# Kernel tuning notes

Hardware: AMD Instinct MI355X
Metric: run time of the kernel (lower is better)

Reference implementation:

```python
import jax, jax.numpy as jnp
import numpy as np

B, C_IN, S = 32, 4, 2048
NF = 256          # CNN filters
H = 256           # LSTM hidden per direction
NH, DH = 8, 64    # heads, single-head size
MH = 512          # multihead size
KSZ, PAD, POOL = 13, 6, 6
SP = (S + 2 * PAD - KSZ + 1) // POOL  # 341: post conv(len-preserving)+maxpool1d length


def _lstm_dir(x, Wih, Whh, b):
    # x: [T, N, C] -- torch LSTM gate order i,f,g,o; b = b_ih + b_hh merged
    N = x.shape[1]
    h0 = jnp.zeros((N, H), x.dtype)
    c0 = jnp.zeros((N, H), x.dtype)

    def step(carry, xt):
        h, c = carry
        g = xt @ Wih.T + h @ Whh.T + b
        i, f, gg, o = jnp.split(g, 4, axis=-1)
        c = jax.nn.sigmoid(f) * c + jax.nn.sigmoid(i) * jnp.tanh(gg)
        h = jax.nn.sigmoid(o) * jnp.tanh(c)
        return (h, c), h

    _, hs = jax.lax.scan(step, (h0, c0), x)
    return hs


def _bilstm(x, Wih, Whh, b):
    fwd = _lstm_dir(x, Wih[0], Whh[0], b[0])
    bwd = _lstm_dir(x[::-1], Wih[1], Whh[1], b[1])[::-1]
    return jnp.concatenate([fwd, bwd], axis=-1)


def _rpe():
    # RelativePosition: |clip(k-q, -(S-1), S-1)| / (S-1); identical across the
    # batch-repeat channels, so compute once then broadcast (same math).
    r = jnp.arange(S)
    d = jnp.abs(jnp.clip(r[None, :] - r[:, None], -(S - 1), S - 1))
    d = d.astype(jnp.float32) / jnp.float32(S - 1)
    # nn.MaxPool2d((9,9), stride=(6,6), padding=1) -> [341, 341]
    return jax.lax.reduce_window(d, -jnp.inf, jax.lax.max, (9, 9), (6, 6), [(1, 1), (1, 1)])


def setup_inputs():
    key = jax.random.key(0)
    ks = jax.random.split(key, 20)
    f = lambda i, shape: jax.random.normal(ks[i], shape, jnp.float32) * 0.05
    return {
        "inputs": jax.random.normal(ks[0], (B, C_IN, S), jnp.float32),
        "conv1_w": f(1, (NF, C_IN, KSZ)),
        "bn1_gamma": jnp.ones((NF,), jnp.float32),
        "bn1_beta": jnp.zeros((NF,), jnp.float32),
        "Wih0": f(2, (2, 4 * H, NF)),
        "Whh0": f(3, (2, 4 * H, H)),
        "b0": f(4, (2, 4 * H)),
        "Wih1": f(5, (2, 4 * H, 2 * H)),
        "Whh1": f(6, (2, 4 * H, H)),
        "b1": f(7, (2, 4 * H)),
        "Qw": f(8, (NH, DH, 2 * H)), "Qb": f(9, (NH, DH)),
        "Kw": f(10, (NH, DH, 2 * H)), "Kb": f(11, (NH, DH)),
        "Vw": f(12, (NH, DH, 2 * H)), "Vb": f(13, (NH, DH)),
        "mh_w": f(14, (MH, NH * DH)), "mh_b": f(15, (MH,)),
    }


def reference(inputs, conv1_w, bn1_gamma, bn1_beta, Wih0, Whh0, b0,
              Wih1, Whh1, b1, Qw, Qb, Kw, Kb, Vw, Vb, mh_w, mh_b):
    # layer1: Conv1d (bias=False, pad=6 keeps length) + BatchNorm1d(eval: mean=0, var=1) + ReLU + MaxPool1d(6)
    x = jax.lax.conv_general_dilated(inputs, conv1_w, (1,), [(PAD, PAD)],
                                     dimension_numbers=('NCH', 'OIH', 'NCH'))
    x = x * (bn1_gamma / jnp.sqrt(1.0 + 1e-5))[None, :, None] + bn1_beta[None, :, None]
    x = jax.nn.relu(x)
    x = jax.lax.reduce_window(x, -jnp.inf, jax.lax.max, (1, 1, POOL), (1, 1, POOL), 'VALID')  # [B,NF,SP]
    x = jnp.transpose(x, (0, 2, 1))  # [B, SP, NF]

    # torch nn.LSTM with batch_first=False fed [B,SP,NF]: scans over axis 0 (batch) -- replicated faithfully.
    x = _bilstm(x, Wih0, Whh0, b0)
    x = _bilstm(x, Wih1, Whh1, b1)  # [B, SP, 2H]
    # (the F_RNN/R_RNN split-and-concat is an identity)

    # per-head Q/K/V (batched over heads), relative attention, dropout off (eval)
    q = jnp.einsum('bsc,hdc->hbsd', x, Qw) + Qb[:, None, None, :]
    k = jnp.einsum('bsc,hdc->hbsd', x, Kw) + Kb[:, None, None, :]
    v = jnp.einsum('bsc,hdc->hbsd', x, Vw) + Vb[:, None, None, :]
    scores = jnp.einsum('hbqd,hbkd->hbqk', q, k) / jnp.sqrt(jnp.float32(DH))
    scores = scores / _rpe()[None, None, :, :]
    p = jax.nn.softmax(scores, axis=-1)
    attn = jax.nn.relu(jnp.einsum('hbqk,hbkd->hbqd', p, v))  # [NH,B,SP,DH]
    cat = jnp.transpose(attn, (1, 2, 0, 3)).reshape(B, SP, NH * DH)
    out = jax.nn.relu(cat @ mh_w.T + mh_b)  # MultiHeadLinear + MHReLU
    return out
```

## Files before the change

kernel.cpp:

```cpp
#include <hip/hip_runtime.h>
#include <math.h>

#define B_    32
#define CIN   4
#define SLEN  2048
#define NF    256
#define HD    256
#define SP    341
#define RTOT  (B_*SP)
#define NH_   8
#define DH_   64
#define GRP   4
#define HS    (SP*HD)
#define PKS   768
#define BSTR  136

typedef __attribute__((ext_vector_type(8))) short short8;
typedef __attribute__((ext_vector_type(4))) float floatx4;
typedef __attribute__((ext_vector_type(4))) unsigned short ushortx4;
typedef __attribute__((ext_vector_type(8))) unsigned short ushort8;

__device__ __forceinline__ float sigmoidf_(float x) { return 1.0f / (1.0f + expf(-x)); }

__device__ __forceinline__ unsigned short f2bf(float x) {
    unsigned int u = __float_as_uint(x);
    unsigned int r = (u + 0x7FFF + ((u >> 16) & 1)) >> 16;
    return (unsigned short)r;
}
__device__ __forceinline__ float bf2f(unsigned short b) {
    return __uint_as_float(((unsigned int)b) << 16);
}

__device__ __forceinline__ void store_f4_llc(float* p, floatx4 v)
{
    asm volatile("global_store_dwordx4 %0, %1, off sc0 sc1" :: "v"(p), "v"(v) : "memory");
}
__device__ __forceinline__ unsigned load_u32_llc(const unsigned* p)
{
    unsigned r;
    asm volatile("global_load_dword %0, %1, off sc0 sc1\n\ts_waitcnt vmcnt(0)"
                 : "=v"(r) : "v"(p) : "memory");
    return r;
}
__device__ __forceinline__ void load_h16_llc(const float* p, floatx4* r)
{
    asm volatile(
        "global_load_dwordx4 %0, %16, off sc0 sc1\n\t"
        "global_load_dwordx4 %1, %16, off offset:16 sc0 sc1\n\t"
        "global_load_dwordx4 %2, %16, off offset:128 sc0 sc1\n\t"
        "global_load_dwordx4 %3, %16, off offset:144 sc0 sc1\n\t"
        "global_load_dwordx4 %4, %16, off offset:256 sc0 sc1\n\t"
        "global_load_dwordx4 %5, %16, off offset:272 sc0 sc1\n\t"
        "global_load_dwordx4 %6, %16, off offset:384 sc0 sc1\n\t"
        "global_load_dwordx4 %7, %16, off offset:400 sc0 sc1\n\t"
        "global_load_dwordx4 %8, %16, off offset:512 sc0 sc1\n\t"
        "global_load_dwordx4 %9, %16, off offset:528 sc0 sc1\n\t"
        "global_load_dwordx4 %10, %16, off offset:640 sc0 sc1\n\t"
        "global_load_dwordx4 %11, %16, off offset:656 sc0 sc1\n\t"
        "global_load_dwordx4 %12, %16, off offset:768 sc0 sc1\n\t"
        "global_load_dwordx4 %13, %16, off offset:784 sc0 sc1\n\t"
        "global_load_dwordx4 %14, %16, off offset:896 sc0 sc1\n\t"
        "global_load_dwordx4 %15, %16, off offset:912 sc0 sc1\n\t"
        "s_waitcnt vmcnt(0)"
        : "=&v"(r[0]), "=&v"(r[1]), "=&v"(r[2]), "=&v"(r[3]),
          "=&v"(r[4]), "=&v"(r[5]), "=&v"(r[6]), "=&v"(r[7]),
          "=&v"(r[8]), "=&v"(r[9]), "=&v"(r[10]), "=&v"(r[11]),
          "=&v"(r[12]), "=&v"(r[13]), "=&v"(r[14]), "=&v"(r[15])
        : "v"(p)
        : "memory");
}


__global__ __launch_bounds__(256)
void conv_pool_k(const float* __restrict__ in, const float* __restrict__ cw,
                 const float* __restrict__ gamma, const float* __restrict__ beta,
                 unsigned short* __restrict__ x0p)
{
    const int b  = blockIdx.y;
    const int s0 = blockIdx.x * 16;
    const int co = threadIdx.x;
    __shared__ float ins[CIN][16*6 + 12];
    for (int idx = threadIdx.x; idx < CIN*108; idx += 256) {
        int ci = idx / 108, o = idx % 108;
        int pos = 6*s0 - 6 + o;
        ins[ci][o] = (pos >= 0 && pos < SLEN) ? in[(b*CIN + ci)*SLEN + pos] : 0.0f;
    }
    float wreg[52];
    {
        const float4* wp = (const float4*)(cw + co*52);
        #pragma unroll
        for (int j4 = 0; j4 < 13; ++j4) {
            float4 w4 = wp[j4];
            wreg[j4*4+0]=w4.x; wreg[j4*4+1]=w4.y; wreg[j4*4+2]=w4.z; wreg[j4*4+3]=w4.w;
        }
    }
    const float scale = gamma[co] * (1.0f / sqrtf(1.0f + 1e-5f));
    const float shift = beta[co];
    __syncthreads();
    for (int si = 0; si < 16; ++si) {
        int s = s0 + si;
        if (s >= SP) break;
        float win[CIN][18];
        #pragma unroll
        for (int ci = 0; ci < CIN; ++ci)
            #pragma unroll
            for (int o = 0; o < 18; ++o)
                win[ci][o] = ins[ci][6*si + o];
        float m = -1e30f;
        #pragma unroll
        for (int p6 = 0; p6 < 6; ++p6) {
            float acc = 0.0f;
            #pragma unroll
            for (int ci = 0; ci < CIN; ++ci)
                #pragma unroll
                for (int kk = 0; kk < 13; ++kk)
                    acc += win[ci][p6+kk] * wreg[ci*13+kk];
            float val = acc * scale + shift;
            val = fmaxf(val, 0.0f);
            m = fmaxf(m, val);
        }
        unsigned short hb_ = f2bf(m);
        unsigned short lb_ = f2bf(m - bf2f(hb_));
        size_t rb = (size_t)(b*SP + s)*512 + (size_t)(co >> 3)*16 + (co & 7);
        x0p[rb]     = hb_;
        x0p[rb + 8] = lb_;
    }
}

__global__ __launch_bounds__(256)
void pack4_k(const float* __restrict__ W, unsigned short* __restrict__ hi,
             unsigned short* __restrict__ lo, int n4)
{
    int i = blockIdx.x * 256 + threadIdx.x;
    if (i >= n4) return;
    float4 x = *((const float4*)W + i);
    float v[4] = {x.x, x.y, x.z, x.w};
    ushortx4 h, l;
    #pragma unroll
    for (int e = 0; e < 4; ++e) {
        unsigned short hb = f2bf(v[e]);
        h[e] = hb;
        l[e] = f2bf(v[e] - bf2f(hb));
    }
    *((ushortx4*)hi + i) = h;
    *((ushortx4*)lo + i) = l;
}

__global__ __launch_bounds__(256)
void pack8_k(const float* __restrict__ W, unsigned short* __restrict__ O, int n8)
{
    int i = blockIdx.x * 256 + threadIdx.x;
    if (i >= n8) return;
    const float4* wp = (const float4*)W + (size_t)i*2;
    float4 a = wp[0], b = wp[1];
    float v[8] = {a.x,a.y,a.z,a.w,b.x,b.y,b.z,b.w};
    ushort8 h, l;
    #pragma unroll
    for (int e = 0; e < 8; ++e) {
        unsigned short hb = f2bf(v[e]);
        h[e] = hb;
        l[e] = f2bf(v[e] - bf2f(hb));
    }
    *(ushort8*)(O + (size_t)i*16)     = h;
    *(ushort8*)(O + (size_t)i*16 + 8) = l;
}

template<int RELU>
__global__ __launch_bounds__(256)
void gemm_bf_k(const unsigned short* __restrict__ Ap, const unsigned short* __restrict__ Bp,
               const float* __restrict__ bias, float* __restrict__ C,
               int M, int N, int K)
{
    const int n0 = blockIdx.x * 128;
    const int m0 = blockIdx.y * 128;
    const int tid = threadIdx.x;
    const int lane = tid & 63;
    const int w = tid >> 6;
    const int wm = w >> 1, wn = w & 1;
    const int ln15 = lane & 15, lq = lane >> 4;
    const int l8 = lane >> 3, lj = lane & 7;
    const size_t rstr = 2*(size_t)K;

    __shared__ unsigned short As[128*64];
    __shared__ unsigned short Bs[128*64];

    floatx4 acc[4][4];
    #pragma unroll
    for (int i = 0; i < 4; ++i)
        #pragma unroll
        for (int j = 0; j < 4; ++j) acc[i][j] = (floatx4){0.f, 0.f, 0.f, 0.f};

    int rloc[4];
    #pragma unroll
    for (int c = 0; c < 4; ++c) rloc[c] = w*32 + c*8 + l8;
    const int spos = lj ^ (l8 & 7);

    for (int k0 = 0; k0 < K; k0 += 32) {
        short8 va[4], vb[4];
        #pragma unroll
        for (int c = 0; c < 4; ++c) {
            int gra = m0 + rloc[c]; if (gra >= M) gra = M - 1;
            va[c] = *(const short8*)(Ap + (size_t)gra*rstr + k0*2 + lj*8);
            vb[c] = *(const short8*)(Bp + (size_t)(n0 + rloc[c])*rstr + k0*2 + lj*8);
        }
        __syncthreads();
        #pragma unroll
        for (int c = 0; c < 4; ++c) {
            *(short8*)&As[rloc[c]*64 + spos*8] = va[c];
            *(short8*)&Bs[rloc[c]*64 + spos*8] = vb[c];
        }
        __syncthreads();

        short8 fa_h[4], fa_l[4], fb_h[4], fb_l[4];
        #pragma unroll
        for (int mt = 0; mt < 4; ++mt) {
            const int lr = wm*64 + mt*16 + ln15;
            fa_h[mt] = *(const short8*)&As[lr*64 + (((lq*2  ) ^ (lr&7))*8)];
            fa_l[mt] = *(const short8*)&As[lr*64 + (((lq*2+1) ^ (lr&7))*8)];
        }
        #pragma unroll
        for (int nt = 0; nt < 4; ++nt) {
            const int lr = wn*64 + nt*16 + ln15;
            fb_h[nt] = *(const short8*)&Bs[lr*64 + (((lq*2  ) ^ (lr&7))*8)];
            fb_l[nt] = *(const short8*)&Bs[lr*64 + (((lq*2+1) ^ (lr&7))*8)];
        }
        #pragma unroll
        for (int mt = 0; mt < 4; ++mt)
            #pragma unroll
            for (int nt = 0; nt < 4; ++nt) {
                acc[mt][nt] = __builtin_amdgcn_mfma_f32_16x16x32_bf16(fa_l[mt], fb_h[nt], acc[mt][nt], 0, 0, 0);
                acc[mt][nt] = __builtin_amdgcn_mfma_f32_16x16x32_bf16(fa_h[mt], fb_l[nt], acc[mt][nt], 0, 0, 0);
                acc[mt][nt] = __builtin_amdgcn_mfma_f32_16x16x32_bf16(fa_h[mt], fb_h[nt], acc[mt][nt], 0, 0, 0);
            }
    }

    #pragma unroll
    for (int nt = 0; nt < 4; ++nt) {
        const int n = n0 + wn*64 + nt*16 + ln15;
        const float bv = bias[n];
        #pragma unroll
        for (int mt = 0; mt < 4; ++mt) {
            const int mbase = m0 + wm*64 + mt*16 + lq*4;
            #pragma unroll
            for (int r = 0; r < 4; ++r) {
                int m = mbase + r;
                if (m < M) {
                    float val = acc[mt][nt][r] + bv;
                    if (RELU) val = fmaxf(val, 0.0f);
                    C[(size_t)m*N + n] = val;
                }
            }
        }
    }
}

__global__ __launch_bounds__(256)
void lstm_scan_k(const float* __restrict__ G,
                 const unsigned short* __restrict__ Whi,
                 const unsigned short* __restrict__ Wlo,
                 float* __restrict__ hb,
                 unsigned short* __restrict__ x_out,
                 unsigned* __restrict__ bar)
{
    const int j0 = blockIdx.x * 32;
    const int m0 = blockIdx.y * 32;
    const int d  = blockIdx.z;
    const int tid = threadIdx.x;
    const int w = tid >> 6, lane = tid & 63;
    const int mhalf = w & 1, gpair = w >> 1;
    const int ln15 = lane & 15, lq = lane >> 4;
    const size_t hsz = (size_t)2*SP*HD;
    unsigned* gbar = bar + (size_t)(blockIdx.y*2 + blockIdx.z)*64;

    __shared__ float Csh[32][132];

    int am = m0 + mhalf*16 + ln15; if (am > SP-1) am = SP-1;
    const int akoff = lq * 8;

    const unsigned short* WhiD = Whi + (size_t)d*1024*256;
    const unsigned short* WloD = Wlo + (size_t)d*1024*256;
    int nrow[4];
    #pragma unroll
    for (int t = 0; t < 4; ++t)
        nrow[t] = (gpair*2 + (t>>1))*256 + j0 + (t&1)*16 + ln15;

    const int emloc = tid >> 3;
    const int ej4   = (tid & 7) * 4;
    const int em    = m0 + emloc;

    floatx4 creg = (floatx4){0.f, 0.f, 0.f, 0.f};

    for (int s = 0; s < B_; ++s) {
        const int t_in = d ? (B_ - 1 - s) : s;
        float* hbuf_in  = hb + (size_t)(s & 1)*hsz;
        float* hbuf_out = hb + (size_t)((s+1) & 1)*hsz;

        floatx4 acc[4];
        #pragma unroll
        for (int t = 0; t < 4; ++t) acc[t] = (floatx4){0.f, 0.f, 0.f, 0.f};

        if (s > 0) {
            const float* p = hbuf_in + (size_t)d*HS + (size_t)am*HD + akoff;
            floatx4 hr[16];
            load_h16_llc(p, hr);
            #pragma unroll
            for (int kk = 0; kk < 8; ++kk) {
                const int ko = kk*32 + akoff;
                float vv[8] = {hr[2*kk][0], hr[2*kk][1], hr[2*kk][2], hr[2*kk][3],
                               hr[2*kk+1][0], hr[2*kk+1][1], hr[2*kk+1][2], hr[2*kk+1][3]};
                short8 ahi, alo;
                #pragma unroll
                for (int e = 0; e < 8; ++e) {
                    unsigned short hb16 = f2bf(vv[e]);
                    ahi[e] = (short)hb16;
                    alo[e] = (short)f2bf(vv[e] - bf2f(hb16));
                }
                #pragma unroll
                for (int t = 0; t < 4; ++t) {
                    short8 bhi = *(const short8*)(WhiD + (size_t)nrow[t]*HD + ko);
                    short8 blo = *(const short8*)(WloD + (size_t)nrow[t]*HD + ko);
                    acc[t] = __builtin_amdgcn_mfma_f32_16x16x32_bf16(alo, bhi, acc[t], 0, 0, 0);
                    acc[t] = __builtin_amdgcn_mfma_f32_16x16x32_bf16(ahi, blo, acc[t], 0, 0, 0);
                    acc[t] = __builtin_amdgcn_mfma_f32_16x16x32_bf16(ahi, bhi, acc[t], 0, 0, 0);
                }
            }
        }

        #pragma unroll
        for (int t = 0; t < 4; ++t) {
            int col = gpair*64 + (t>>1)*32 + (t&1)*16 + ln15;
            int rb  = mhalf*16 + lq*4;
            #pragma unroll
            for (int r = 0; r < 4; ++r)
                Csh[rb + r][col] = acc[t][r];
        }
        __syncthreads();

        if (em < SP) {
            size_t gb = ((size_t)t_in*SP + em)*2048 + (size_t)d*1024 + j0 + ej4;
            float4 gi4 = *(const float4*)&G[gb];
            float4 gf4 = *(const float4*)&G[gb + 256];
            float4 gg4 = *(const float4*)&G[gb + 512];
            float4 go4 = *(const float4*)&G[gb + 768];
            float hv[4];
            #pragma unroll
            for (int e = 0; e < 4; ++e) {
                float gi = Csh[emloc][     ej4+e] + (&gi4.x)[e];
                float gf = Csh[emloc][32 + ej4+e] + (&gf4.x)[e];
                float gg = Csh[emloc][64 + ej4+e] + (&gg4.x)[e];
                float go = Csh[emloc][96 + ej4+e] + (&go4.x)[e];
                float cn = sigmoidf_(gf)*creg[e] + sigmoidf_(gi)*tanhf(gg);
                creg[e] = cn;
                hv[e] = sigmoidf_(go)*tanhf(cn);
            }
            size_t cbase = ((size_t)d*SP + em)*HD + j0 + ej4;
            floatx4 ho = (floatx4){hv[0], hv[1], hv[2], hv[3]};
            store_f4_llc(&hbuf_out[cbase], ho);
            const int colg = d*HD + j0 + ej4;
            size_t xb = ((size_t)t_in*SP + em)*1024 + (size_t)(colg >> 3)*16 + (colg & 7);
            ushortx4 xh, xl;
            #pragma unroll
            for (int e = 0; e < 4; ++e) {
                unsigned short hb16 = f2bf(hv[e]);
                xh[e] = hb16;
                xl[e] = f2bf(hv[e] - bf2f(hb16));
            }
            *(ushortx4*)&x_out[xb]     = xh;
            *(ushortx4*)&x_out[xb + 8] = xl;
        }

        if (s < B_ - 1) {
            asm volatile("s_waitcnt vmcnt(0)" ::: "memory");
            __syncthreads();
            if (tid == 0) {
                atomicAdd(gbar, 1u);
                const unsigned target = (unsigned)(s + 1) * 8u;
                while (load_u32_llc(gbar) < target)
                    __builtin_amdgcn_s_sleep(2);
            }
            __syncthreads();
        }
    }
}

__global__ __launch_bounds__(256)
void scores_sm_k(const float* __restrict__ q, const float* __restrict__ k,
                 unsigned short* __restrict__ Ppk, int g)
{
    const int h = blockIdx.z, bl = blockIdx.y, bg = g*GRP + bl;
    const int q0 = blockIdx.x * 32;
    const int tid = threadIdx.x;
    const int tx = tid & 15, ty = tid >> 4;
    __shared__ float qs[32][68];
    __shared__ float ks[64][68];
    {
        int jr = tid >> 3, c8 = (tid & 7) * 8;
        int qq = q0 + jr; if (qq > SP-1) qq = SP-1;
        const float* qp = &q[((size_t)bg*SP + qq)*512 + h*64 + c8];
        *(float4*)&qs[jr][c8]     = *(const float4*)qp;
        *(float4*)&qs[jr][c8 + 4] = *(const float4*)(qp + 4);
    }
    float sv[2][24];
    for (int kc = 0; kc < 6; ++kc) {
        __syncthreads();
        {
            int jr = tid >> 2, c16 = (tid & 3) * 16;
            int kr = kc*64 + jr; if (kr > SP-1) kr = SP-1;
            const float* kp = &k[((size_t)bg*SP + kr)*512 + h*64 + c16];
            #pragma unroll
            for (int u = 0; u < 4; ++u)
                *(float4*)&ks[jr][c16 + u*4] = *(const float4*)(kp + u*4);
        }
        __syncthreads();
        float a_[2][4] = {{0.f,0.f,0.f,0.f},{0.f,0.f,0.f,0.f}};
        for (int d4 = 0; d4 < 64; d4 += 4) {
            float4 a0 = *(const float4*)&qs[ty][d4];
            float4 a1 = *(const float4*)&qs[ty + 16][d4];
            float4 b[4];
            #pragma unroll
            for (int j = 0; j < 4; ++j) b[j] = *(const float4*)&ks[tx + 16*j][d4];
            #pragma unroll
            for (int j = 0; j < 4; ++j) {
                a_[0][j] += a0.x*b[j].x + a0.y*b[j].y + a0.z*b[j].z + a0.w*b[j].w;
                a_[1][j] += a1.x*b[j].x + a1.y*b[j].y + a1.z*b[j].z + a1.w*b[j].w;
            }
        }
        #pragma unroll
        for (int i = 0; i < 2; ++i)
            #pragma unroll
            for (int j = 0; j < 4; ++j) sv[i][kc*4 + j] = a_[i][j];
    }
    #pragma unroll
    for (int i = 0; i < 2; ++i) {
        const int qq = q0 + ty + 16*i;
        int r0 = 6*qq - 1; if (r0 < 0) r0 = 0;
        int r1 = 6*qq + 7; if (r1 > SLEN-1) r1 = SLEN-1;
        float m = -1e30f;
        #pragma unroll
        for (int jj = 0; jj < 24; ++jj) {
            const int col = (jj >> 2)*64 + (jj & 3)*16 + tx;
            float s;
            if (col < SP) {
                int c0 = 6*col - 1; if (c0 < 0) c0 = 0;
                int c1 = 6*col + 7;
                int dd1 = c1 - r0; if (dd1 < 0) dd1 = -dd1;
                int dd2 = r1 - c0; if (dd2 < 0) dd2 = -dd2;
                int den = dd1 > dd2 ? dd1 : dd2;
                s = (sv[i][jj] * 0.125f) * 2047.0f / (float)den;
            } else s = -1e30f;
            sv[i][jj] = s;
            m = fmaxf(m, s);
        }
        #pragma unroll
        for (int o = 1; o < 16; o <<= 1) m = fmaxf(m, __shfl_xor(m, o, 64));
        float sum = 0.0f;
        #pragma unroll
        for (int jj = 0; jj < 24; ++jj) {
            float v = expf(sv[i][jj] - m);
            sv[i][jj] = v;
            sum += v;
        }
        #pragma unroll
        for (int o = 1; o < 16; o <<= 1) sum += __shfl_xor(sum, o, 64);
        const float inv = 1.0f / sum;
        if (qq < SP) {
            const size_t pb = ((size_t)(h*GRP + bl)*SP + qq) * PKS;
            #pragma unroll
            for (int jj = 0; jj < 24; ++jj) {
                const int col = (jj >> 2)*64 + (jj & 3)*16 + tx;
                float p = sv[i][jj] * inv;
                unsigned short hb16 = f2bf(p);
                size_t pp = pb + (size_t)((col >> 3)*16 + (col & 7));
                Ppk[pp]     = hb16;
                Ppk[pp + 8] = f2bf(p - bf2f(hb16));
            }
        }
    }
}

__global__ __launch_bounds__(256)
void pv_bf_k(const unsigned short* __restrict__ Ppk, const float* __restrict__ vbuf,
             unsigned short* __restrict__ catp, int g)
{
    const int h = blockIdx.z, bl = blockIdx.y, bg = g*GRP + bl;
    const int q0 = blockIdx.x * 64;
    const int tid = threadIdx.x;
    const int lane = tid & 63, w = tid >> 6;
    const int ln15 = lane & 15, lq = lane >> 4;
    __shared__ unsigned short As[64][BSTR];
    __shared__ unsigned short Bs[64][BSTR];
    floatx4 acc[4];
    #pragma unroll
    for (int nt = 0; nt < 4; ++nt) acc[nt] = (floatx4){0.f,0.f,0.f,0.f};
    const size_t prow = (size_t)(h*GRP + bl)*SP;
    const int sr = tid >> 2;
    const int sa = (tid & 3) * 32;
    const int sd = (tid & 3) * 16;

    for (int chunk = 0; chunk < 6; ++chunk) {
        int qa = q0 + sr; if (qa > SP-1) qa = SP-1;
        const unsigned short* ap = Ppk + (prow + qa)*PKS + chunk*128 + sa;
        short8 a0 = *(const short8*)ap;
        short8 a1 = *(const short8*)(ap + 8);
        short8 a2 = *(const short8*)(ap + 16);
        short8 a3 = *(const short8*)(ap + 24);
        const int kr = chunk*64 + sr;
        float vv[16];
        if (kr < SP) {
            const float* vp = &vbuf[((size_t)bg*SP + kr)*512 + h*64 + sd];
            *(float4*)&vv[0]  = ((const float4*)vp)[0];
            *(float4*)&vv[4]  = ((const float4*)vp)[1];
            *(float4*)&vv[8]  = ((const float4*)vp)[2];
            *(float4*)&vv[12] = ((const float4*)vp)[3];
        } else {
            #pragma unroll
            for (int e = 0; e < 16; ++e) vv[e] = 0.0f;
        }
        __syncthreads();
        *(short8*)&As[sr][sa]      = a0;
        *(short8*)&As[sr][sa + 8]  = a1;
        *(short8*)&As[sr][sa + 16] = a2;
        *(short8*)&As[sr][sa + 24] = a3;
        {
            const int c = (sr >> 3)*16 + (sr & 7);
            #pragma unroll
            for (int e = 0; e < 16; ++e) {
                unsigned short hb16 = f2bf(vv[e]);
                Bs[sd + e][c]     = hb16;
                Bs[sd + e][c + 8] = f2bf(vv[e] - bf2f(hb16));
            }
        }
        __syncthreads();
        #pragma unroll
        for (int s = 0; s < 2; ++s) {
            const int ko = s*64 + lq*16;
            short8 fa_h = *(const short8*)&As[w*16 + ln15][ko];
            short8 fa_l = *(const short8*)&As[w*16 + ln15][ko + 8];
            #pragma unroll
            for (int nt = 0; nt < 4; ++nt) {
                short8 fb_h = *(const short8*)&Bs[nt*16 + ln15][ko];
                short8 fb_l = *(const short8*)&Bs[nt*16 + ln15][ko + 8];
                acc[nt] = __builtin_amdgcn_mfma_f32_16x16x32_bf16(fa_l, fb_h, acc[nt], 0, 0, 0);
                acc[nt] = __builtin_amdgcn_mfma_f32_16x16x32_bf16(fa_h, fb_l, acc[nt], 0, 0, 0);
                acc[nt] = __builtin_amdgcn_mfma_f32_16x16x32_bf16(fa_h, fb_h, acc[nt], 0, 0, 0);
            }
        }
    }
    #pragma unroll
    for (int nt = 0; nt < 4; ++nt) {
        const int colg = h*64 + nt*16 + ln15;
        #pragma unroll
        for (int r = 0; r < 4; ++r) {
            const int em = q0 + w*16 + lq*4 + r;
            if (em < SP) {
                float val = fmaxf(acc[nt][r], 0.0f);
                size_t xb = ((size_t)bg*SP + em)*1024 + (size_t)((colg >> 3)*16 + (colg & 7));
                unsigned short hb16 = f2bf(val);
                catp[xb]     = hb16;
                catp[xb + 8] = f2bf(val - bf2f(hb16));
            }
        }
    }
}

extern "C" void kernel_launch(void* const* d_in, const int* in_sizes, int n_in,
                              void* d_out, int out_size, void* d_ws, size_t ws_size,
                              hipStream_t stream)
{
    (void)in_sizes; (void)n_in; (void)out_size; (void)ws_size;
    const float* in    = (const float*)d_in[0];
    const float* cw    = (const float*)d_in[1];
    const float* gamma = (const float*)d_in[2];
    const float* beta  = (const float*)d_in[3];
    const float* Wih0  = (const float*)d_in[4];
    const float* Whh0  = (const float*)d_in[5];
    const float* b0    = (const float*)d_in[6];
    const float* Wih1  = (const float*)d_in[7];
    const float* Whh1  = (const float*)d_in[8];
    const float* b1    = (const float*)d_in[9];
    const float* Qw    = (const float*)d_in[10];
    const float* Qb    = (const float*)d_in[11];
    const float* Kw    = (const float*)d_in[12];
    const float* Kb    = (const float*)d_in[13];
    const float* Vw    = (const float*)d_in[14];
    const float* Vb    = (const float*)d_in[15];
    const float* mhw   = (const float*)d_in[16];
    const float* mhb   = (const float*)d_in[17];
    float* out = (float*)d_out;

    float* x0 = (float*)d_ws;
    float* G  = x0 + (size_t)RTOT*NF;
    float* x1 = G  + (size_t)RTOT*2048;
    float* x2 = x1 + (size_t)RTOT*512;
    float* hb = x2 + (size_t)RTOT*512;
    float* cb = hb + (size_t)2*2*SP*HD;

    float* qbuf = G;
    float* kbuf = G + (size_t)RTOT*512;
    float* vbuf = G + (size_t)2*RTOT*512;
    unsigned short* Ppk = (unsigned short*)(G + (size_t)3*RTOT*512);
    unsigned* bar = (unsigned*)cb;

    unsigned short* x0p = (unsigned short*)x0;
    unsigned short* whh1_hi = (unsigned short*)x0;
    unsigned short* whh1_lo = whh1_hi + (size_t)524288;
    unsigned short* qw_p = (unsigned short*)(x0 + (size_t)524288);
    unsigned short* kw_p = qw_p + (size_t)524288;
    unsigned short* vw_p = kw_p + (size_t)524288;
    unsigned short* mw_p = vw_p + (size_t)524288;
    unsigned short* wih0_p  = (unsigned short*)x2;
    unsigned short* wih1_p  = wih0_p + (size_t)1048576;
    unsigned short* whh0_hi = wih1_p + (size_t)2097152;
    unsigned short* whh0_lo = whh0_hi + (size_t)524288;
    unsigned short* x1p  = (unsigned short*)x1;
    unsigned short* catp = (unsigned short*)x1;
    unsigned short* x2p = (unsigned short*)x2;

    #define PACKGRID(n) dim3(((n) + 255) / 256)

    conv_pool_k<<<dim3(22, B_), 256, 0, stream>>>(in, cw, gamma, beta, x0p);
    pack8_k<<<PACKGRID(65536), 256, 0, stream>>>(Wih0, wih0_p, 65536);
    gemm_bf_k<0><<<dim3(16, 86), 256, 0, stream>>>(x0p, wih0_p, b0, G, RTOT, 2048, 256);
    pack4_k<<<PACKGRID(131072), 256, 0, stream>>>(Whh0, whh0_hi, whh0_lo, 131072);
    pack4_k<<<PACKGRID(131072), 256, 0, stream>>>(Whh1, whh1_hi, whh1_lo, 131072);
    pack8_k<<<PACKGRID(131072), 256, 0, stream>>>(Wih1, wih1_p, 131072);
    hipMemsetAsync(bar, 0, 22*64*sizeof(unsigned), stream);
    {
        const float* a0 = G; const unsigned short* a1 = whh0_hi; const unsigned short* a2 = whh0_lo;
        float* a3 = hb; unsigned short* a4 = x1p; unsigned* a5 = bar;
        void* kargs[] = {&a0, &a1, &a2, &a3, &a4, &a5};
        hipLaunchCooperativeKernel((void*)lstm_scan_k, dim3(8, 11, 2), dim3(256, 1, 1), kargs, 0, stream);
    }
    gemm_bf_k<0><<<dim3(16, 86), 256, 0, stream>>>(x1p, wih1_p, b1, G, RTOT, 2048, 512);
    hipMemsetAsync(bar, 0, 22*64*sizeof(unsigned), stream);
    {
        const float* a0 = G; const unsigned short* a1 = whh1_hi; const unsigned short* a2 = whh1_lo;
        float* a3 = hb; unsigned short* a4 = x2p; unsigned* a5 = bar;
        void* kargs[] = {&a0, &a1, &a2, &a3, &a4, &a5};
        hipLaunchCooperativeKernel((void*)lstm_scan_k, dim3(8, 11, 2), dim3(256, 1, 1), kargs, 0, stream);
    }
    pack8_k<<<PACKGRID(32768), 256, 0, stream>>>(Qw,  qw_p, 32768);
    pack8_k<<<PACKGRID(32768), 256, 0, stream>>>(Kw,  kw_p, 32768);
    pack8_k<<<PACKGRID(32768), 256, 0, stream>>>(Vw,  vw_p, 32768);
    pack8_k<<<PACKGRID(32768), 256, 0, stream>>>(mhw, mw_p, 32768);
    gemm_bf_k<0><<<dim3(4, 86), 256, 0, stream>>>(x2p, qw_p, Qb, qbuf, RTOT, 512, 512);
    gemm_bf_k<0><<<dim3(4, 86), 256, 0, stream>>>(x2p, kw_p, Kb, kbuf, RTOT, 512, 512);
    gemm_bf_k<0><<<dim3(4, 86), 256, 0, stream>>>(x2p, vw_p, Vb, vbuf, RTOT, 512, 512);
    for (int g = 0; g < B_/GRP; ++g) {
        scores_sm_k<<<dim3(11, GRP, NH_), 256, 0, stream>>>(qbuf, kbuf, Ppk, g);
        pv_bf_k    <<<dim3(6,  GRP, NH_), 256, 0, stream>>>(Ppk, vbuf, catp, g);
    }
    gemm_bf_k<1><<<dim3(4, 86), 256, 0, stream>>>(catp, mw_p, mhb, out, RTOT, 512, 512);
    #undef PACKGRID
}
```

Measured before the change: 1.697 ms.

## Fuse scores, softmax and PV into one attention kernel over all batches

Replaces the per-group scores_sm_k and pv_bf_k launch pairs (16 launches) with a single attn_k over the full batch. The kernel keeps softmax probabilities in shared memory, which removes the packed bf16 hi/lo probability buffer and its global round trip. PV is now computed with fp32 FMAs from LDS instead of split-bf16 MFMA. Tiles shrink to 16 queries per block, so K and V are reloaded more often and the PV step runs on scalar FP32 ALUs rather than matrix cores.

```diff
diff --git a/kernel.cpp b/kernel.cpp
--- a/kernel.cpp
+++ b/kernel.cpp
@@ -10,10 +10,8 @@
 #define RTOT  (B_*SP)
 #define NH_   8
 #define DH_   64
-#define GRP   4
 #define HS    (SP*HD)
-#define PKS   768
-#define BSTR  136
+#define SSTR  388
 
 typedef __attribute__((ext_vector_type(8))) short short8;
 typedef __attribute__((ext_vector_type(4))) float floatx4;
@@ -384,23 +382,24 @@
 }
 
 __global__ __launch_bounds__(256)
-void scores_sm_k(const float* __restrict__ q, const float* __restrict__ k,
-                 unsigned short* __restrict__ Ppk, int g)
-{
-    const int h = blockIdx.z, bl = blockIdx.y, bg = g*GRP + bl;
-    const int q0 = blockIdx.x * 32;
+void attn_k(const float* __restrict__ q, const float* __restrict__ k,
+            const float* __restrict__ v, unsigned short* __restrict__ catp)
+{
+    const int h = blockIdx.z, bg = blockIdx.y;
+    const int q0 = blockIdx.x * 16;
     const int tid = threadIdx.x;
     const int tx = tid & 15, ty = tid >> 4;
-    __shared__ float qs[32][68];
-    __shared__ float ks[64][68];
+    __shared__ float qs[16][68];
+    __shared__ float st[64][68];
+    __shared__ float S[16][SSTR];
+
     {
-        int jr = tid >> 3, c8 = (tid & 7) * 8;
+        int jr = tid >> 4, c4 = (tid & 15) * 4;
         int qq = q0 + jr; if (qq > SP-1) qq = SP-1;
-        const float* qp = &q[((size_t)bg*SP + qq)*512 + h*64 + c8];
-        *(float4*)&qs[jr][c8]     = *(const float4*)qp;
-        *(float4*)&qs[jr][c8 + 4] = *(const float4*)(qp + 4);
-    }
-    float sv[2][24];
+        *(float4*)&qs[jr][c4] = *(const float4*)&q[((size_t)bg*SP + qq)*512 + h*64 + c4];
+    }
+
+    float sv[24];
     for (int kc = 0; kc < 6; ++kc) {
         __syncthreads();
         {
@@ -409,30 +408,25 @@
             const float* kp = &k[((size_t)bg*SP + kr)*512 + h*64 + c16];
             #pragma unroll
             for (int u = 0; u < 4; ++u)
-                *(float4*)&ks[jr][c16 + u*4] = *(const float4*)(kp + u*4);
-        }
-        __syncthreads();
-        float a_[2][4] = {{0.f,0.f,0.f,0.f},{0.f,0.f,0.f,0.f}};
+                *(float4*)&st[jr][c16 + u*4] = *(const float4*)(kp + u*4);
+        }
+        __syncthreads();
+        float a_[4] = {0.f, 0.f, 0.f, 0.f};
         for (int d4 = 0; d4 < 64; d4 += 4) {
             float4 a0 = *(const float4*)&qs[ty][d4];
-            float4 a1 = *(const float4*)&qs[ty + 16][d4];
             float4 b[4];
             #pragma unroll
-            for (int j = 0; j < 4; ++j) b[j] = *(const float4*)&ks[tx + 16*j][d4];
-            #pragma unroll
-            for (int j = 0; j < 4; ++j) {
-                a_[0][j] += a0.x*b[j].x + a0.y*b[j].y + a0.z*b[j].z + a0.w*b[j].w;
-                a_[1][j] += a1.x*b[j].x + a1.y*b[j].y + a1.z*b[j].z + a1.w*b[j].w;
-            }
-        }
-        #pragma unroll
-        for (int i = 0; i < 2; ++i)
-            #pragma unroll
-            for (int j = 0; j < 4; ++j) sv[i][kc*4 + j] = a_[i][j];
-    }
-    #pragma unroll
-    for (int i = 0; i < 2; ++i) {
-        const int qq = q0 + ty + 16*i;
+            for (int j = 0; j < 4; ++j) b[j] = *(const float4*)&st[tx + 16*j][d4];
+            #pragma unroll
+            for (int j = 0; j < 4; ++j)
+                a_[j] += a0.x*b[j].x + a0.y*b[j].y + a0.z*b[j].z + a0.w*b[j].w;
+        }
+        #pragma unroll
+        for (int j = 0; j < 4; ++j) sv[kc*4 + j] = a_[j];
+    }
+
+    {
+        const int qq = q0 + ty;
         int r0 = 6*qq - 1; if (r0 < 0) r0 = 0;
         int r1 = 6*qq + 7; if (r1 > SLEN-1) r1 = SLEN-1;
         float m = -1e30f;
@@ -446,9 +440,9 @@
                 int dd1 = c1 - r0; if (dd1 < 0) dd1 = -dd1;
                 int dd2 = r1 - c0; if (dd2 < 0) dd2 = -dd2;
                 int den = dd1 > dd2 ? dd1 : dd2;
-                s = (sv[i][jj] * 0.125f) * 2047.0f / (float)den;
+                s = (sv[jj] * 0.125f) * 2047.0f / (float)den;
             } else s = -1e30f;
-            sv[i][jj] = s;
+            sv[jj] = s;
             m = fmaxf(m, s);
         }
         #pragma unroll
@@ -456,110 +450,54 @@
         float sum = 0.0f;
         #pragma unroll
         for (int jj = 0; jj < 24; ++jj) {
-            float v = expf(sv[i][jj] - m);
-            sv[i][jj] = v;
-            sum += v;
+            float vv_ = expf(sv[jj] - m);
+            sv[jj] = vv_;
+            sum += vv_;
         }
         #pragma unroll
         for (int o = 1; o < 16; o <<= 1) sum += __shfl_xor(sum, o, 64);
         const float inv = 1.0f / sum;
-        if (qq < SP) {
-            const size_t pb = ((size_t)(h*GRP + bl)*SP + qq) * PKS;
-            #pragma unroll
-            for (int jj = 0; jj < 24; ++jj) {
-                const int col = (jj >> 2)*64 + (jj & 3)*16 + tx;
-                float p = sv[i][jj] * inv;
-                unsigned short hb16 = f2bf(p);
-                size_t pp = pb + (size_t)((col >> 3)*16 + (col & 7));
-                Ppk[pp]     = hb16;
-                Ppk[pp + 8] = f2bf(p - bf2f(hb16));
-            }
-        }
-    }
-}
-
-__global__ __launch_bounds__(256)
-void pv_bf_k(const unsigned short* __restrict__ Ppk, const float* __restrict__ vbuf,
-             unsigned short* __restrict__ catp, int g)
-{
-    const int h = blockIdx.z, bl = blockIdx.y, bg = g*GRP + bl;
-    const int q0 = blockIdx.x * 64;
-    const int tid = threadIdx.x;
-    const int lane = tid & 63, w = tid >> 6;
-    const int ln15 = lane & 15, lq = lane >> 4;
-    __shared__ unsigned short As[64][BSTR];
-    __shared__ unsigned short Bs[64][BSTR];
-    floatx4 acc[4];
-    #pragma unroll
-    for (int nt = 0; nt < 4; ++nt) acc[nt] = (floatx4){0.f,0.f,0.f,0.f};
-    const size_t prow = (size_t)(h*GRP + bl)*SP;
-    const int sr = tid >> 2;
-    const int sa = (tid & 3) * 32;
-    const int sd = (tid & 3) * 16;
-
-    for (int chunk = 0; chunk < 6; ++chunk) {
-        int qa = q0 + sr; if (qa > SP-1) qa = SP-1;
-        const unsigned short* ap = Ppk + (prow + qa)*PKS + chunk*128 + sa;
-        short8 a0 = *(const short8*)ap;
-        short8 a1 = *(const short8*)(ap + 8);
-        short8 a2 = *(const short8*)(ap + 16);
-        short8 a3 = *(const short8*)(ap + 24);
-        const int kr = chunk*64 + sr;
-        float vv[16];
-        if (kr < SP) {
-            const float* vp = &vbuf[((size_t)bg*SP + kr)*512 + h*64 + sd];
-            *(float4*)&vv[0]  = ((const float4*)vp)[0];
-            *(float4*)&vv[4]  = ((const float4*)vp)[1];
-            *(float4*)&vv[8]  = ((const float4*)vp)[2];
-            *(float4*)&vv[12] = ((const float4*)vp)[3];
-        } else {
-            #pragma unroll
-            for (int e = 0; e < 16; ++e) vv[e] = 0.0f;
-        }
-        __syncthreads();
-        *(short8*)&As[sr][sa]      = a0;
-        *(short8*)&As[sr][sa + 8]  = a1;
-        *(short8*)&As[sr][sa + 16] = a2;
-        *(short8*)&As[sr][sa + 24] = a3;
+        #pragma unroll
+        for (int jj = 0; jj < 24; ++jj) {
+            const int col = (jj >> 2)*64 + (jj & 3)*16 + tx;
+            S[ty][col] = sv[jj] * inv;
+        }
+    }
+    __syncthreads();
+
+    float o[4] = {0.f, 0.f, 0.f, 0.f};
+    for (int kc = 0; kc < 6; ++kc) {
         {
-            const int c = (sr >> 3)*16 + (sr & 7);
-            #pragma unroll
-            for (int e = 0; e < 16; ++e) {
-                unsigned short hb16 = f2bf(vv[e]);
-                Bs[sd + e][c]     = hb16;
-                Bs[sd + e][c + 8] = f2bf(vv[e] - bf2f(hb16));
-            }
-        }
-        __syncthreads();
-        #pragma unroll
-        for (int s = 0; s < 2; ++s) {
-            const int ko = s*64 + lq*16;
-            short8 fa_h = *(const short8*)&As[w*16 + ln15][ko];
-            short8 fa_l = *(const short8*)&As[w*16 + ln15][ko + 8];
-            #pragma unroll
-            for (int nt = 0; nt < 4; ++nt) {
-                short8 fb_h = *(const short8*)&Bs[nt*16 + ln15][ko];
-                short8 fb_l = *(const short8*)&Bs[nt*16 + ln15][ko + 8];
-                acc[nt] = __builtin_amdgcn_mfma_f32_16x16x32_bf16(fa_l, fb_h, acc[nt], 0, 0, 0);
-                acc[nt] = __builtin_amdgcn_mfma_f32_16x16x32_bf16(fa_h, fb_l, acc[nt], 0, 0, 0);
-                acc[nt] = __builtin_amdgcn_mfma_f32_16x16x32_bf16(fa_h, fb_h, acc[nt], 0, 0, 0);
-            }
-        }
-    }
-    #pragma unroll
-    for (int nt = 0; nt < 4; ++nt) {
-        const int colg = h*64 + nt*16 + ln15;
-        #pragma unroll
-        for (int r = 0; r < 4; ++r) {
-            const int em = q0 + w*16 + lq*4 + r;
-            if (em < SP) {
-                float val = fmaxf(acc[nt][r], 0.0f);
-                size_t xb = ((size_t)bg*SP + em)*1024 + (size_t)((colg >> 3)*16 + (colg & 7));
-                unsigned short hb16 = f2bf(val);
-                catp[xb]     = hb16;
-                catp[xb + 8] = f2bf(val - bf2f(hb16));
-            }
-        }
+            int jr = tid >> 2, c16 = (tid & 3) * 16;
+            int kr = kc*64 + jr; if (kr > SP-1) kr = SP-1;
+            const float* vp = &v[((size_t)bg*SP + kr)*512 + h*64 + c16];
+            #pragma unroll
+            for (int u = 0; u < 4; ++u)
+                *(float4*)&st[jr][c16 + u*4] = *(const float4*)(vp + u*4);
+        }
+        __syncthreads();
+        for (int kk = 0; kk < 64; ++kk) {
+            float p = S[ty][kc*64 + kk];
+            float4 vv = *(const float4*)&st[kk][tx*4];
+            o[0] += p*vv.x; o[1] += p*vv.y; o[2] += p*vv.z; o[3] += p*vv.w;
+        }
+        __syncthreads();
+    }
+
+    const int em = q0 + ty;
+    if (em < SP) {
+        const int colg = h*64 + tx*4;
+        size_t xb = ((size_t)bg*SP + em)*1024 + (size_t)((colg >> 3)*16 + (colg & 7));
+        ushortx4 xh, xl;
+        #pragma unroll
+        for (int e = 0; e < 4; ++e) {
+            float val = fmaxf(o[e], 0.0f);
+            unsigned short hb16 = f2bf(val);
+            xh[e] = hb16;
+            xl[e] = f2bf(val - bf2f(hb16));
+        }
+        *(ushortx4*)&catp[xb]     = xh;
+        *(ushortx4*)&catp[xb + 8] = xl;
     }
 }
 
@@ -598,7 +536,6 @@
     float* qbuf = G;
     float* kbuf = G + (size_t)RTOT*512;
     float* vbuf = G + (size_t)2*RTOT*512;
-    unsigned short* Ppk = (unsigned short*)(G + (size_t)3*RTOT*512);
     unsigned* bar = (unsigned*)cb;
 
     unsigned short* x0p = (unsigned short*)x0;
@@ -646,10 +583,7 @@
     gemm_bf_k<0><<<dim3(4, 86), 256, 0, stream>>>(x2p, qw_p, Qb, qbuf, RTOT, 512, 512);
     gemm_bf_k<0><<<dim3(4, 86), 256, 0, stream>>>(x2p, kw_p, Kb, kbuf, RTOT, 512, 512);
     gemm_bf_k<0><<<dim3(4, 86), 256, 0, stream>>>(x2p, vw_p, Vb, vbuf, RTOT, 512, 512);
-    for (int g = 0; g < B_/GRP; ++g) {
-        scores_sm_k<<<dim3(11, GRP, NH_), 256, 0, stream>>>(qbuf, kbuf, Ppk, g);
-        pv_bf_k    <<<dim3(6,  GRP, NH_), 256, 0, stream>>>(Ppk, vbuf, catp, g);
-    }
+    attn_k<<<dim3(22, B_, NH_), 256, 0, stream>>>(qbuf, kbuf, vbuf, catp);
     gemm_bf_k<1><<<dim3(4, 86), 256, 0, stream>>>(catp, mw_p, mhb, out, RTOT, 512, 512);
     #undef PACKGRID
 }
```

New measurement: 1.583 ms. 6.7% less time.
